# Kernel tuning notes

Hardware: AMD Instinct MI355X
Metric: run time of the kernel (lower is better)

The kernel has to match this reference:

```python
import jax, jax.numpy as jnp
import numpy as np

D = 1024
H = 16
DFF = 4096
EPS = 1e-5


def layernorm(x, g, b):
    m = jnp.mean(x, axis=-1, keepdims=True)
    v = jnp.var(x, axis=-1, keepdims=True)
    return (x - m) * jax.lax.rsqrt(v + EPS) * g + b


def setup_inputs() -> dict:
    key = jax.random.key(0)
    ks = jax.random.split(key, 6)
    B, T = 2, 2048
    s = 0.02
    return {
        "x": jax.random.normal(ks[0], (B, T, D), dtype=jnp.float32),
        "W_qkv": jax.random.normal(ks[1], (D, 3 * D), dtype=jnp.float32) * s,
        "W_proj": jax.random.normal(ks[2], (D, D), dtype=jnp.float32) * s,
        "W_fc1": jax.random.normal(ks[3], (D, DFF), dtype=jnp.float32) * s,
        "W_fc2": jax.random.normal(ks[4], (DFF, D), dtype=jnp.float32) * s,
        "ln1_g": jnp.ones((D,), jnp.float32),
        "ln1_b": jnp.zeros((D,), jnp.float32),
        "ln2_g": jnp.ones((D,), jnp.float32),
        "ln2_b": jnp.zeros((D,), jnp.float32),
    }


def reference(x, W_qkv, W_proj, W_fc1, W_fc2, ln1_g, ln1_b, ln2_g, ln2_b):
    B, T, C = x.shape
    hd = C // H

    # --- attention sublayer (pre-norm) ---
    h = layernorm(x, ln1_g, ln1_b)
    qkv = h @ W_qkv                                  # [B,T,3C]
    q, k, v = jnp.split(qkv, 3, axis=-1)
    q = q.reshape(B, T, H, hd).transpose(0, 2, 1, 3)  # [B,H,T,hd]
    k = k.reshape(B, T, H, hd).transpose(0, 2, 1, 3)
    v = v.reshape(B, T, H, hd).transpose(0, 2, 1, 3)
    att = jnp.einsum('bhqd,bhkd->bhqk', q, k) * (1.0 / np.sqrt(hd))
    causal = jnp.tril(jnp.ones((T, T), dtype=bool))
    att = jnp.where(causal, att, jnp.float32(-jnp.inf))
    att = jax.nn.softmax(att, axis=-1)
    y = jnp.einsum('bhqk,bhkd->bhqd', att, v)        # [B,H,T,hd]
    y = y.transpose(0, 2, 1, 3).reshape(B, T, C)
    x = x + y @ W_proj

    # --- MLP sublayer (pre-norm) ---
    h = layernorm(x, ln2_g, ln2_b)
    h = jax.nn.gelu(h @ W_fc1, approximate=False)
    x = x + h @ W_fc2
    return x
```

## Files before the change

### kernel.cpp

```cpp
#include <hip/hip_runtime.h>
#include <hip/hip_bf16.h>
#include <math.h>

typedef __bf16 bf16;
typedef __bf16 bf16x4 __attribute__((ext_vector_type(4)));
typedef __bf16 bf16x8 __attribute__((ext_vector_type(8)));
typedef float f32x4 __attribute__((ext_vector_type(4)));
typedef unsigned int u32;

#define MFMA_BF16(a, b, c) __builtin_amdgcn_mfma_f32_16x16x32_bf16(a, b, c, 0, 0, 0)
#define ASYNC16(g, l)                                                                   \
    __builtin_amdgcn_global_load_lds((const __attribute__((address_space(1))) u32*)(g), \
                                     (__attribute__((address_space(3))) u32*)(l), 16, 0, 0)

__global__ __launch_bounds__(256)
void transpose_cast(const float* __restrict__ in, bf16* __restrict__ out, int rows, int cols) {
    __shared__ float tile[32][33];
    const int tx = threadIdx.x, ty = threadIdx.y;
    const int c0 = blockIdx.x * 32, r0 = blockIdx.y * 32;
    #pragma unroll
    for (int j = 0; j < 4; j++)
        tile[ty + j * 8][tx] = in[(size_t)(r0 + ty + j * 8) * cols + c0 + tx];
    __syncthreads();
    #pragma unroll
    for (int j = 0; j < 4; j++)
        out[(size_t)(c0 + ty + j * 8) * rows + r0 + tx] = (bf16)tile[tx][ty + j * 8];
}

__global__ __launch_bounds__(256)
void transpose_v(const bf16* __restrict__ qkv, bf16* __restrict__ vt) {
    __shared__ bf16 tile[32][33];
    const int tx = threadIdx.x, ty = threadIdx.y;
    const int t0 = blockIdx.x * 32;
    const int d0 = blockIdx.y * 32;
    const int bh = blockIdx.z;
    const int b = bh >> 4, h = bh & 15;
    const bf16* src = qkv + (size_t)b * 2048 * 3072 + 2048 + h * 64;
    #pragma unroll
    for (int j = 0; j < 4; j++)
        tile[ty + j * 8][tx] = src[(size_t)(t0 + ty + j * 8) * 3072 + d0 + tx];
    __syncthreads();
    #pragma unroll
    for (int j = 0; j < 4; j++)
        vt[((size_t)bh * 64 + d0 + ty + j * 8) * 2048 + t0 + tx] = tile[tx][ty + j * 8];
}

__global__ __launch_bounds__(256)
void ln_kernel(const float* __restrict__ x, const float* __restrict__ g,
               const float* __restrict__ bb, bf16* __restrict__ out) {
    const int row = blockIdx.x, tid = threadIdx.x;
    const float4 v = reinterpret_cast<const float4*>(x)[(size_t)row * 256 + tid];
    float s = v.x + v.y + v.z + v.w;
    float sq = v.x * v.x + v.y * v.y + v.z * v.z + v.w * v.w;
    #pragma unroll
    for (int o = 32; o > 0; o >>= 1) { s += __shfl_xor(s, o); sq += __shfl_xor(sq, o); }
    __shared__ float ssum[4], ssq[4];
    const int wave = tid >> 6, lane = tid & 63;
    if (lane == 0) { ssum[wave] = s; ssq[wave] = sq; }
    __syncthreads();
    s = ssum[0] + ssum[1] + ssum[2] + ssum[3];
    sq = ssq[0] + ssq[1] + ssq[2] + ssq[3];
    const float mean = s * (1.0f / 1024.0f);
    const float var = sq * (1.0f / 1024.0f) - mean * mean;
    const float rstd = rsqrtf(var + 1e-5f);
    const float4 gv = reinterpret_cast<const float4*>(g)[tid];
    const float4 bv = reinterpret_cast<const float4*>(bb)[tid];
    bf16x4 o;
    o[0] = (bf16)((v.x - mean) * rstd * gv.x + bv.x);
    o[1] = (bf16)((v.y - mean) * rstd * gv.y + bv.y);
    o[2] = (bf16)((v.z - mean) * rstd * gv.z + bv.z);
    o[3] = (bf16)((v.w - mean) * rstd * gv.w + bv.w);
    reinterpret_cast<bf16x4*>(out)[(size_t)row * 256 + tid] = o;
}

__device__ __forceinline__ float gelu_fast(float v) {
    const float vv = v * v;
    const float u = v * (1.595769122f + 0.0713548162726f * vv);
    const float t = exp2f(u * -1.4426950408889634f);
    return v / (1.0f + t);
}

template <int EPI>
__global__ __launch_bounds__(512, 2)
void gemm256(const bf16* __restrict__ A, const bf16* __restrict__ Bt,
             bf16* __restrict__ outb, int M, int N, int K) {
    __shared__ bf16 As[2][2][2][128][32];
    __shared__ bf16 Bs[2][2][2][128][32];
    const int tid = threadIdx.x;
    const int wave = tid >> 6, lane = tid & 63;
    const int lm = lane & 15, lq = lane >> 4;
    const int wr = wave >> 2, wc = wave & 3;
    const int bm = blockIdx.y * 256, bn = blockIdx.x * 256;
    const int srow = lane >> 2;
    const int sg = (((lane & 3) ^ ((lane >> 3) & 3)) * 8);
    const int pco = (lq ^ ((lm >> 1) & 3)) * 8;

    f32x4 acc[8][4];
    #pragma unroll
    for (int i = 0; i < 8; i++)
        #pragma unroll
        for (int j = 0; j < 4; j++) acc[i][j] = (f32x4){0.f, 0.f, 0.f, 0.f};

    auto stageA = [&](int db, int kt) {
        #pragma unroll
        for (int L = 0; L < 2; L++) {
            const int g = wave * 2 + L, slab = g >> 3, rg = g & 7;
            #pragma unroll
            for (int h = 0; h < 2; h++)
                ASYNC16(A + (size_t)(bm + h * 128 + rg * 16 + srow) * K + kt + slab * 32 + sg,
                        &As[db][h][slab][rg * 16][0]);
        }
    };
    auto stageB = [&](int db, int kt) {
        #pragma unroll
        for (int L = 0; L < 2; L++) {
            const int g = wave * 2 + L, slab = g >> 3, rg = g & 7;
            #pragma unroll
            for (int h = 0; h < 2; h++)
                ASYNC16(Bt + (size_t)(bn + h * 128 + rg * 16 + srow) * K + kt + slab * 32 + sg,
                        &Bs[db][h][slab][rg * 16][0]);
        }
    };
    auto loadA = [&](int db, int mq, bf16x8 (&dst)[4][2]) {
        #pragma unroll
        for (int i = 0; i < 4; i++)
            #pragma unroll
            for (int kk = 0; kk < 2; kk++)
                dst[i][kk] = *reinterpret_cast<const bf16x8*>(
                    &As[db][wr][kk][(mq * 4 + i) * 16 + lm][pco]);
    };
    auto loadB = [&](int db, int bq, bf16x8 (&dst)[2][2]) {
        #pragma unroll
        for (int j = 0; j < 2; j++)
            #pragma unroll
            for (int kk = 0; kk < 2; kk++)
                dst[j][kk] = *reinterpret_cast<const bf16x8*>(
                    &Bs[db][wc >> 1][kk][(wc & 1) * 64 + (bq * 2 + j) * 16 + lm][pco]);
    };
    auto quad = [&](int mq, int bq, bf16x8 (&a)[4][2], bf16x8 (&b)[2][2]) {
        #pragma unroll
        for (int kk = 0; kk < 2; kk++)
            #pragma unroll
            for (int i = 0; i < 4; i++)
                #pragma unroll
                for (int j = 0; j < 2; j++)
                    acc[mq * 4 + i][bq * 2 + j] =
                        MFMA_BF16(a[i][kk], b[j][kk], acc[mq * 4 + i][bq * 2 + j]);
    };

#define PHASE_SYNC()                                         \
    __builtin_amdgcn_s_barrier();                            \
    asm volatile("s_waitcnt lgkmcnt(0)" ::: "memory");       \
    __builtin_amdgcn_sched_barrier(0)

    const int NT = K >> 6;
    stageB(0, 0);  stageA(0, 0);
    stageB(1, 64); stageA(1, 64);
    asm volatile("s_waitcnt vmcnt(8)" ::: "memory");
    __builtin_amdgcn_s_barrier();
    __builtin_amdgcn_sched_barrier(0);

    bf16x8 af[4][2], b0[2][2], b1[2][2];
    for (int t = 0; t < NT; ++t) {
        const int db = t & 1;
        const int kt2 = (t + 2) * 64;
        loadA(db, 0, af);
        loadB(db, 0, b0);
        PHASE_SYNC();
        __builtin_amdgcn_s_setprio(1);
        quad(0, 0, af, b0);
        __builtin_amdgcn_s_setprio(0);
        __builtin_amdgcn_s_barrier();
        loadB(db, 1, b1);
        PHASE_SYNC();
        __builtin_amdgcn_s_setprio(1);
        quad(0, 1, af, b1);
        __builtin_amdgcn_s_setprio(0);
        __builtin_amdgcn_s_barrier();
        loadA(db, 1, af);
        if (t + 2 < NT) stageB(db, kt2);
        PHASE_SYNC();
        __builtin_amdgcn_s_setprio(1);
        quad(1, 0, af, b0);
        __builtin_amdgcn_s_setprio(0);
        __builtin_amdgcn_s_barrier();
        if (t + 2 < NT) {
            stageA(db, kt2);
            asm volatile("s_waitcnt vmcnt(8)" ::: "memory");
        } else if (t + 1 < NT) {
            asm volatile("s_waitcnt vmcnt(0)" ::: "memory");
        }
        __builtin_amdgcn_s_barrier();
        __builtin_amdgcn_sched_barrier(0);
        __builtin_amdgcn_s_setprio(1);
        quad(1, 1, af, b1);
        __builtin_amdgcn_s_setprio(0);
        __builtin_amdgcn_s_barrier();
    }
#undef PHASE_SYNC

    const int r0 = bm + wr * 128, c0 = bn + wc * 64;
    #pragma unroll
    for (int mi = 0; mi < 8; mi++)
        #pragma unroll
        for (int ni = 0; ni < 4; ni++)
            #pragma unroll
            for (int e = 0; e < 4; e++) {
                const int row = r0 + mi * 16 + lq * 4 + e;
                const int col = c0 + ni * 16 + lm;
                const float v = acc[mi][ni][e];
                const size_t idx = (size_t)row * N + col;
                if (EPI == 0) outb[idx] = (bf16)v;
                else          outb[idx] = (bf16)gelu_fast(v);
            }
}

__global__ __launch_bounds__(512, 2)
void gemm128p(const bf16* __restrict__ A, const bf16* __restrict__ Bt,
              const float* __restrict__ resid, float* __restrict__ outf,
              int M, int N, int K) {
    __shared__ bf16 As[3][128][64];
    __shared__ bf16 Bs[3][128][64];
    const int tid = threadIdx.x;
    const int wave = tid >> 6, lane = tid & 63;
    const int lm = lane & 15, lq = lane >> 4;
    const int wm = (wave >> 2) * 64, wn = (wave & 3) * 32;
    const int bm = blockIdx.y * 128, bn = blockIdx.x * 128;
    const int lr8 = lane >> 3;
    const int lg  = ((lane & 7) ^ lr8) * 8;
    const int sa  = lm & 7;
    int co[2];
    co[0] = (lq ^ sa) * 8;
    co[1] = ((lq ^ 4) ^ sa) * 8;
    f32x4 acc[4][2];
    #pragma unroll
    for (int i = 0; i < 4; i++)
        #pragma unroll
        for (int j = 0; j < 2; j++) acc[i][j] = (f32x4){0.f, 0.f, 0.f, 0.f};

    auto stageA = [&](int s, int kt) {
        #pragma unroll
        for (int c = 0; c < 2; c++)
            ASYNC16(A + (size_t)(bm + (wave * 2 + c) * 8 + lr8) * K + kt + lg,
                    &As[s][(wave * 2 + c) * 8][0]);
    };
    auto stageB = [&](int s, int kt) {
        #pragma unroll
        for (int c = 0; c < 2; c++)
            ASYNC16(Bt + (size_t)(bn + (wave * 2 + c) * 8 + lr8) * K + kt + lg,
                    &Bs[s][(wave * 2 + c) * 8][0]);
    };

    const int NT = K >> 6;
    stageA(0, 0);  stageB(0, 0);
    stageA(1, 64); stageB(1, 64);
    asm volatile("s_waitcnt vmcnt(4)" ::: "memory");
    __builtin_amdgcn_s_barrier();
    __builtin_amdgcn_sched_barrier(0);

    int s = 0;
    for (int t = 0; t < NT; ++t) {
        const int s2 = (s + 2 >= 3) ? s - 1 : s + 2;
        const int kt2 = (t + 2) * 64;
        bf16x8 a0[4], b0[2];
        #pragma unroll
        for (int mi = 0; mi < 4; mi++)
            a0[mi] = *reinterpret_cast<const bf16x8*>(&As[s][wm + mi * 16 + lm][co[0]]);
        #pragma unroll
        for (int nj = 0; nj < 2; nj++)
            b0[nj] = *reinterpret_cast<const bf16x8*>(&Bs[s][wn + nj * 16 + lm][co[0]]);
        if (t + 2 < NT) stageA(s2, kt2);
        __builtin_amdgcn_s_barrier();
        asm volatile("s_waitcnt lgkmcnt(0)" ::: "memory");
        __builtin_amdgcn_sched_barrier(0);
        __builtin_amdgcn_s_setprio(1);
        #pragma unroll
        for (int mi = 0; mi < 4; mi++)
            #pragma unroll
            for (int nj = 0; nj < 2; nj++)
                acc[mi][nj] = MFMA_BF16(a0[mi], b0[nj], acc[mi][nj]);
        __builtin_amdgcn_s_setprio(0);
        __builtin_amdgcn_s_barrier();
        #pragma unroll
        for (int mi = 0; mi < 4; mi++)
            a0[mi] = *reinterpret_cast<const bf16x8*>(&As[s][wm + mi * 16 + lm][co[1]]);
        #pragma unroll
        for (int nj = 0; nj < 2; nj++)
            b0[nj] = *reinterpret_cast<const bf16x8*>(&Bs[s][wn + nj * 16 + lm][co[1]]);
        if (t + 2 < NT) {
            stageB(s2, kt2);
            asm volatile("s_waitcnt vmcnt(4)" ::: "memory");
        } else if (t + 1 < NT) {
            asm volatile("s_waitcnt vmcnt(0)" ::: "memory");
        }
        __builtin_amdgcn_s_barrier();
        asm volatile("s_waitcnt lgkmcnt(0)" ::: "memory");
        __builtin_amdgcn_sched_barrier(0);
        __builtin_amdgcn_s_setprio(1);
        #pragma unroll
        for (int mi = 0; mi < 4; mi++)
            #pragma unroll
            for (int nj = 0; nj < 2; nj++)
                acc[mi][nj] = MFMA_BF16(a0[mi], b0[nj], acc[mi][nj]);
        __builtin_amdgcn_s_setprio(0);
        __builtin_amdgcn_s_barrier();
        s = (s == 2) ? 0 : s + 1;
    }

    const int r0 = bm + wm, c0 = bn + wn;
    #pragma unroll
    for (int i = 0; i < 4; i++)
        #pragma unroll
        for (int j = 0; j < 2; j++)
            #pragma unroll
            for (int e = 0; e < 4; e++) {
                const int row = r0 + i * 16 + lq * 4 + e;
                const int col = c0 + j * 16 + lm;
                const size_t idx = (size_t)row * N + col;
                outf[idx] = resid[idx] + acc[i][j][e];
            }
}

__global__ __launch_bounds__(256)
void attn_kernel(const bf16* __restrict__ qkv, const bf16* __restrict__ vt,
                 bf16* __restrict__ y) {
    __shared__ bf16 Ks[64][68];
    __shared__ bf16 Vt[64][68];
    __shared__ bf16 Ps[4][16][68];
    const int tid = threadIdx.x, wave = tid >> 6, lane = tid & 63;
    const int lm = lane & 15, lq = lane >> 4;
    const int h = blockIdx.y, b = blockIdx.z;
    const size_t base = (size_t)b * 2048 * 3072;
    const bf16* Kbase = qkv + base + 1024 + h * 64;
    const bf16* Vbase = vt + ((size_t)(b * 16 + h) * 64) * 2048;
    const int skey = tid >> 3, sch = (tid & 7) * 8;
    const float k1 = 0.18033688011112042f;

    bf16x8 ones;
    #pragma unroll
    for (int j = 0; j < 8; j++) ones[j] = (lm == 0) ? (bf16)1.0f : (bf16)0.0f;

    for (int ph = 0; ph < 2; ph++) {
        const int qt = ph ? (int)blockIdx.x : 31 - (int)blockIdx.x;

        const int qrow = qt * 64 + wave * 16 + lm;
        const bf16* qp = qkv + base + (size_t)qrow * 3072 + h * 64 + lq * 8;
        bf16x8 aq0 = *reinterpret_cast<const bf16x8*>(qp);
        bf16x8 aq1 = *reinterpret_cast<const bf16x8*>(qp + 32);
        #pragma unroll
        for (int j = 0; j < 8; j++) {
            aq0[j] = (bf16)((float)aq0[j] * k1);
            aq1[j] = (bf16)((float)aq1[j] * k1);
        }

        f32x4 Oc[4], Ol;
        #pragma unroll
        for (int nt = 0; nt < 4; nt++) Oc[nt] = (f32x4){0.f, 0.f, 0.f, 0.f};
        Ol = (f32x4){0.f, 0.f, 0.f, 0.f};

        bf16x8 pk0, pk1, pv0, pv1;
        {
            const bf16* kp = Kbase + (size_t)skey * 3072 + sch;
            pk0 = *reinterpret_cast<const bf16x8*>(kp);
            pk1 = *reinterpret_cast<const bf16x8*>(kp + (size_t)32 * 3072);
            const bf16* vp = Vbase + (size_t)skey * 2048 + sch;
            pv0 = *reinterpret_cast<const bf16x8*>(vp);
            pv1 = *reinterpret_cast<const bf16x8*>(vp + (size_t)32 * 2048);
        }

        for (int kt2 = 0; kt2 <= qt; kt2++) {
            __syncthreads();
            *reinterpret_cast<bf16x8*>(&Ks[skey][sch])      = pk0;
            *reinterpret_cast<bf16x8*>(&Ks[skey + 32][sch]) = pk1;
            *reinterpret_cast<bf16x8*>(&Vt[skey][sch])      = pv0;
            *reinterpret_cast<bf16x8*>(&Vt[skey + 32][sch]) = pv1;
            __syncthreads();
            if (kt2 < qt) {
                const bf16* kp = Kbase + (size_t)((kt2 + 1) * 64 + skey) * 3072 + sch;
                pk0 = *reinterpret_cast<const bf16x8*>(kp);
                pk1 = *reinterpret_cast<const bf16x8*>(kp + (size_t)32 * 3072);
                const bf16* vp = Vbase + (size_t)skey * 2048 + (kt2 + 1) * 64 + sch;
                pv0 = *reinterpret_cast<const bf16x8*>(vp);
                pv1 = *reinterpret_cast<const bf16x8*>(vp + (size_t)32 * 2048);
            }

            f32x4 Sc[4];
            #pragma unroll
            for (int nt = 0; nt < 4; nt++) Sc[nt] = (f32x4){0.f, 0.f, 0.f, 0.f};
            #pragma unroll
            for (int nt = 0; nt < 4; nt++) {
                const bf16x8 bk0 = *reinterpret_cast<const bf16x8*>(&Ks[nt * 16 + lm][lq * 8]);
                const bf16x8 bk1 = *reinterpret_cast<const bf16x8*>(&Ks[nt * 16 + lm][32 + lq * 8]);
                Sc[nt] = MFMA_BF16(aq0, bk0, Sc[nt]);
                Sc[nt] = MFMA_BF16(aq1, bk1, Sc[nt]);
            }

            const int qb = wave * 16 + lq * 4;
            #pragma unroll
            for (int e = 0; e < 4; e++) {
                #pragma unroll
                for (int nt = 0; nt < 4; nt++) {
                    float sv = Sc[nt][e];
                    if (kt2 == qt && (nt * 16 + lm) > (qb + e)) sv = -1e30f;
                    Ps[wave][lq * 4 + e][nt * 16 + lm] = (bf16)exp2f(sv);
                }
            }

            const bf16x8 ap0 = *reinterpret_cast<const bf16x8*>(&Ps[wave][lm][lq * 8]);
            const bf16x8 ap1 = *reinterpret_cast<const bf16x8*>(&Ps[wave][lm][32 + lq * 8]);
            Ol = MFMA_BF16(ap0, ones, Ol);
            Ol = MFMA_BF16(ap1, ones, Ol);
            #pragma unroll
            for (int nt = 0; nt < 4; nt++) {
                const bf16x8 bv0 = *reinterpret_cast<const bf16x8*>(&Vt[nt * 16 + lm][lq * 8]);
                const bf16x8 bv1 = *reinterpret_cast<const bf16x8*>(&Vt[nt * 16 + lm][32 + lq * 8]);
                Oc[nt] = MFMA_BF16(ap0, bv0, Oc[nt]);
                Oc[nt] = MFMA_BF16(ap1, bv1, Oc[nt]);
            }
        }

        const int qrow0 = qt * 64 + wave * 16 + lq * 4;
        float inv[4];
        #pragma unroll
        for (int e = 0; e < 4; e++) inv[e] = 1.0f / __shfl(Ol[e], lane & 48);
        #pragma unroll
        for (int nt = 0; nt < 4; nt++)
            #pragma unroll
            for (int e = 0; e < 4; e++) {
                const int row = qrow0 + e;
                y[((size_t)b * 2048 + row) * 1024 + h * 64 + nt * 16 + lm] = (bf16)(Oc[nt][e] * inv[e]);
            }
    }
}

extern "C" void kernel_launch(void* const* d_in, const int* in_sizes, int n_in,
                              void* d_out, int out_size, void* d_ws, size_t ws_size,
                              hipStream_t stream) {
    const float* x     = (const float*)d_in[0];
    const float* Wqkv  = (const float*)d_in[1];
    const float* Wproj = (const float*)d_in[2];
    const float* Wfc1  = (const float*)d_in[3];
    const float* Wfc2  = (const float*)d_in[4];
    const float* ln1g  = (const float*)d_in[5];
    const float* ln1b  = (const float*)d_in[6];
    const float* ln2g  = (const float*)d_in[7];
    const float* ln2b  = (const float*)d_in[8];
    float* out = (float*)d_out;
    char* ws = (char*)d_ws;

    bf16*  Wqkvt  = (bf16*)(ws);
    bf16*  Wprojt = (bf16*)(ws + 6291456);
    bf16*  Wfc1t  = (bf16*)(ws + 8388608);
    bf16*  Wfc2t  = (bf16*)(ws + 16777216);
    bf16*  hb     = (bf16*)(ws + 25165824);
    bf16*  vt     = (bf16*)(ws + 25165824);
    bf16*  qkv    = (bf16*)(ws + 33554432);
    bf16*  yb     = (bf16*)(ws + 58720256);
    float* x1     = (float*)(ws + 67108864);
    bf16*  h3     = (bf16*)(ws + 33554432);

    const dim3 tb(32, 8);
    transpose_cast<<<dim3(96, 32), tb, 0, stream>>>(Wqkv, Wqkvt, 1024, 3072);
    transpose_cast<<<dim3(32, 32), tb, 0, stream>>>(Wproj, Wprojt, 1024, 1024);
    transpose_cast<<<dim3(128, 32), tb, 0, stream>>>(Wfc1, Wfc1t, 1024, 4096);
    transpose_cast<<<dim3(32, 128), tb, 0, stream>>>(Wfc2, Wfc2t, 4096, 1024);

    ln_kernel<<<dim3(4096), dim3(256), 0, stream>>>(x, ln1g, ln1b, hb);
    gemm256<0><<<dim3(12, 16), dim3(512), 0, stream>>>(hb, Wqkvt, qkv, 4096, 3072, 1024);
    transpose_v<<<dim3(64, 2, 32), tb, 0, stream>>>(qkv, vt);
    attn_kernel<<<dim3(16, 16, 2), dim3(256), 0, stream>>>(qkv, vt, yb);
    gemm128p<<<dim3(8, 32), dim3(512), 0, stream>>>(yb, Wprojt, x, x1, 4096, 1024, 1024);
    ln_kernel<<<dim3(4096), dim3(256), 0, stream>>>(x1, ln2g, ln2b, hb);
    gemm256<2><<<dim3(16, 16), dim3(512), 0, stream>>>(hb, Wfc1t, h3, 4096, 4096, 1024);
    gemm128p<<<dim3(8, 32), dim3(512), 0, stream>>>(h3, Wfc2t, x1, out, 4096, 1024, 4096);
}
```

Baseline: 342.1 us.

## Split-K the FC2 GEMM with 256-tile kernel and atomic accumulation

Replaces the 128x128-tile FC2 GEMM (K=4096) with a new 256x256-tile kernel split four ways along K. Partial sums are atomically added into the output, which is first seeded with the residual through a device-to-device copy. The aim is to use the larger, more efficient tile while still launching enough blocks (4x16x4 = 256) to fill the CUs. The cost is 4x atomic float traffic on the output, an extra 16 MB copy, and non-deterministic summation order.

```diff
diff --git a/kernel.cpp b/kernel.cpp
--- a/kernel.cpp
+++ b/kernel.cpp
@@ -216,6 +216,138 @@
 }
 
 __global__ __launch_bounds__(512, 2)
+void gemm256sk(const bf16* __restrict__ A, const bf16* __restrict__ Bt,
+               float* __restrict__ outf, int M, int N, int K, int klen) {
+    __shared__ bf16 As[2][2][2][128][32];
+    __shared__ bf16 Bs[2][2][2][128][32];
+    const int tid = threadIdx.x;
+    const int wave = tid >> 6, lane = tid & 63;
+    const int lm = lane & 15, lq = lane >> 4;
+    const int wr = wave >> 2, wc = wave & 3;
+    const int bm = blockIdx.y * 256, bn = blockIdx.x * 256;
+    const int kbase = blockIdx.z * klen;
+    const int srow = lane >> 2;
+    const int sg = (((lane & 3) ^ ((lane >> 3) & 3)) * 8);
+    const int pco = (lq ^ ((lm >> 1) & 3)) * 8;
+
+    f32x4 acc[8][4];
+    #pragma unroll
+    for (int i = 0; i < 8; i++)
+        #pragma unroll
+        for (int j = 0; j < 4; j++) acc[i][j] = (f32x4){0.f, 0.f, 0.f, 0.f};
+
+    auto stageA = [&](int db, int kt) {
+        #pragma unroll
+        for (int L = 0; L < 2; L++) {
+            const int g = wave * 2 + L, slab = g >> 3, rg = g & 7;
+            #pragma unroll
+            for (int h = 0; h < 2; h++)
+                ASYNC16(A + (size_t)(bm + h * 128 + rg * 16 + srow) * K + kbase + kt + slab * 32 + sg,
+                        &As[db][h][slab][rg * 16][0]);
+        }
+    };
+    auto stageB = [&](int db, int kt) {
+        #pragma unroll
+        for (int L = 0; L < 2; L++) {
+            const int g = wave * 2 + L, slab = g >> 3, rg = g & 7;
+            #pragma unroll
+            for (int h = 0; h < 2; h++)
+                ASYNC16(Bt + (size_t)(bn + h * 128 + rg * 16 + srow) * K + kbase + kt + slab * 32 + sg,
+                        &Bs[db][h][slab][rg * 16][0]);
+        }
+    };
+    auto loadA = [&](int db, int mq, bf16x8 (&dst)[4][2]) {
+        #pragma unroll
+        for (int i = 0; i < 4; i++)
+            #pragma unroll
+            for (int kk = 0; kk < 2; kk++)
+                dst[i][kk] = *reinterpret_cast<const bf16x8*>(
+                    &As[db][wr][kk][(mq * 4 + i) * 16 + lm][pco]);
+    };
+    auto loadB = [&](int db, int bq, bf16x8 (&dst)[2][2]) {
+        #pragma unroll
+        for (int j = 0; j < 2; j++)
+            #pragma unroll
+            for (int kk = 0; kk < 2; kk++)
+                dst[j][kk] = *reinterpret_cast<const bf16x8*>(
+                    &Bs[db][wc >> 1][kk][(wc & 1) * 64 + (bq * 2 + j) * 16 + lm][pco]);
+    };
+    auto quad = [&](int mq, int bq, bf16x8 (&a)[4][2], bf16x8 (&b)[2][2]) {
+        #pragma unroll
+        for (int kk = 0; kk < 2; kk++)
+            #pragma unroll
+            for (int i = 0; i < 4; i++)
+                #pragma unroll
+                for (int j = 0; j < 2; j++)
+                    acc[mq * 4 + i][bq * 2 + j] =
+                        MFMA_BF16(a[i][kk], b[j][kk], acc[mq * 4 + i][bq * 2 + j]);
+    };
+
+#define PHASE_SYNC()                                         \
+    __builtin_amdgcn_s_barrier();                            \
+    asm volatile("s_waitcnt lgkmcnt(0)" ::: "memory");       \
+    __builtin_amdgcn_sched_barrier(0)
+
+    const int NT = klen >> 6;
+    stageB(0, 0);  stageA(0, 0);
+    stageB(1, 64); stageA(1, 64);
+    asm volatile("s_waitcnt vmcnt(8)" ::: "memory");
+    __builtin_amdgcn_s_barrier();
+    __builtin_amdgcn_sched_barrier(0);
+
+    bf16x8 af[4][2], b0[2][2], b1[2][2];
+    for (int t = 0; t < NT; ++t) {
+        const int db = t & 1;
+        const int kt2 = (t + 2) * 64;
+        loadA(db, 0, af);
+        loadB(db, 0, b0);
+        PHASE_SYNC();
+        __builtin_amdgcn_s_setprio(1);
+        quad(0, 0, af, b0);
+        __builtin_amdgcn_s_setprio(0);
+        __builtin_amdgcn_s_barrier();
+        loadB(db, 1, b1);
+        PHASE_SYNC();
+        __builtin_amdgcn_s_setprio(1);
+        quad(0, 1, af, b1);
+        __builtin_amdgcn_s_setprio(0);
+        __builtin_amdgcn_s_barrier();
+        loadA(db, 1, af);
+        if (t + 2 < NT) stageB(db, kt2);
+        PHASE_SYNC();
+        __builtin_amdgcn_s_setprio(1);
+        quad(1, 0, af, b0);
+        __builtin_amdgcn_s_setprio(0);
+        __builtin_amdgcn_s_barrier();
+        if (t + 2 < NT) {
+            stageA(db, kt2);
+            asm volatile("s_waitcnt vmcnt(8)" ::: "memory");
+        } else if (t + 1 < NT) {
+            asm volatile("s_waitcnt vmcnt(0)" ::: "memory");
+        }
+        __builtin_amdgcn_s_barrier();
+        __builtin_amdgcn_sched_barrier(0);
+        __builtin_amdgcn_s_setprio(1);
+        quad(1, 1, af, b1);
+        __builtin_amdgcn_s_setprio(0);
+        __builtin_amdgcn_s_barrier();
+    }
+#undef PHASE_SYNC
+
+    const int r0 = bm + wr * 128, c0 = bn + wc * 64;
+    #pragma unroll
+    for (int mi = 0; mi < 8; mi++)
+        #pragma unroll
+        for (int ni = 0; ni < 4; ni++)
+            #pragma unroll
+            for (int e = 0; e < 4; e++) {
+                const int row = r0 + mi * 16 + lq * 4 + e;
+                const int col = c0 + ni * 16 + lm;
+                atomicAdd(&outf[(size_t)row * N + col], acc[mi][ni][e]);
+            }
+}
+
+__global__ __launch_bounds__(512, 2)
 void gemm128p(const bf16* __restrict__ A, const bf16* __restrict__ Bt,
               const float* __restrict__ resid, float* __restrict__ outf,
               int M, int N, int K) {
@@ -472,5 +604,6 @@
     gemm128p<<<dim3(8, 32), dim3(512), 0, stream>>>(yb, Wprojt, x, x1, 4096, 1024, 1024);
     ln_kernel<<<dim3(4096), dim3(256), 0, stream>>>(x1, ln2g, ln2b, hb);
     gemm256<2><<<dim3(16, 16), dim3(512), 0, stream>>>(hb, Wfc1t, h3, 4096, 4096, 1024);
-    gemm128p<<<dim3(8, 32), dim3(512), 0, stream>>>(h3, Wfc2t, x1, out, 4096, 1024, 4096);
-}
+    hipMemcpyAsync(out, x1, 16777216, hipMemcpyDeviceToDevice, stream);
+    gemm256sk<<<dim3(4, 16, 4), dim3(512), 0, stream>>>(h3, Wfc2t, out, 4096, 1024, 4096, 1024);
+}
```

Result: slower. 375.8 us (+9.8%).
